# Kernel tuning notes

Hardware: AMD Instinct MI355X
Metric: run time of the kernel (lower is better)

The kernel has to match this reference:

```python
import jax, jax.numpy as jnp
import numpy as np

N, E, G = 100000, 1600000, 1000
D_IN, D, L, C = 128, 300, 5, 10


def setup_inputs() -> dict:
    key = jax.random.key(0)
    ks = jax.random.split(key, 32)
    s = 0.05
    inp = {
        'x': jax.random.normal(ks[0], (N, D_IN), jnp.float32),
        'edge_index': jax.random.randint(ks[1], (2, E), 0, N, jnp.int64),
        'batch': jnp.sort(jax.random.randint(ks[2], (N,), 0, G, jnp.int64)),
        'enc_W': jax.random.normal(ks[3], (D_IN, D)) * s,
        'enc_b': jnp.zeros((D,)),
        'eps': jnp.zeros((L,)),
        'cW1': jax.random.normal(ks[4], (L, D, 2 * D)) * s,
        'cb1': jnp.zeros((L, 2 * D)),
        'cbn_s': jnp.ones((L, 2 * D)),
        'cbn_b': jnp.zeros((L, 2 * D)),
        'cW2': jax.random.normal(ks[5], (L, 2 * D, D)) * s,
        'cb2': jnp.zeros((L, D)),
        'bn_s': jnp.ones((L, D)),
        'bn_b': jnp.zeros((L, D)),
        'vn0': jnp.zeros((D,)),
        'vW1': jax.random.normal(ks[6], (L, D, 2 * D)) * s,
        'vb1': jnp.zeros((L, 2 * D)),
        'vbn1_s': jnp.ones((L, 2 * D)),
        'vbn1_b': jnp.zeros((L, 2 * D)),
        'vW2': jax.random.normal(ks[7], (L, 2 * D, D)) * s,
        'vb2': jnp.zeros((L, D)),
        'vbn2_s': jnp.ones((L, D)),
        'vbn2_b': jnp.zeros((L, D)),
        'gW1': jax.random.normal(ks[8], (D, 2 * D)) * s,
        'gb1': jnp.zeros((2 * D,)),
        'gbn_s': jnp.ones((2 * D,)),
        'gbn_b': jnp.zeros((2 * D,)),
        'gW2': jax.random.normal(ks[9], (2 * D, 1)) * s,
        'gb2': jnp.zeros((1,)),
        'pW': jax.random.normal(ks[10], (D, C)) * s,
        'pb': jnp.zeros((C,)),
    }
    return inp


def reference(x, enc_W, enc_b, eps, cW1, cb1, cbn_s, cbn_b, cW2, cb2,
              bn_s, bn_b, vn0, vW1, vb1, vbn1_s, vbn1_b, vW2, vb2,
              vbn2_s, vbn2_b, gW1, gb1, gbn_s, gbn_b, gW2, gb2, pW, pb,
              edge_index, batch):
    src, dst = edge_index[0], edge_index[1]
    n = x.shape[0]
    vn = jnp.broadcast_to(vn0, (G, D))  # virtualnode_embedding(zeros) -> row 0 per graph
    h_list = [x @ enc_W + enc_b]
    for l in range(L):
        hl = h_list[l] + vn[batch]  # virtual-node broadcast gather
        # GIN conv: MLP((1+eps)*h + sum_{j in N(i)} h_j)
        agg = jax.ops.segment_sum(hl[src], dst, num_segments=n)
        t = (1.0 + eps[l]) * hl + agg
        t = jax.nn.relu((t @ cW1[l] + cb1[l]) * cbn_s[l] + cbn_b[l])
        h = (t @ cW2[l] + cb2[l]) * bn_s[l] + bn_b[l]  # layer BN (eval, folded)
        if l < L - 1:
            h = jax.nn.relu(h)  # dropout is identity in eval
        # virtual-node update: global_add_pool + MLP
        vtmp = jax.ops.segment_sum(hl, batch, num_segments=G) + vn
        u = jax.nn.relu((vtmp @ vW1[l] + vb1[l]) * vbn1_s[l] + vbn1_b[l])
        vn = jax.nn.relu((u @ vW2[l] + vb2[l]) * vbn2_s[l] + vbn2_b[l])
        h_list.append(h)
    # JK = 'max' across all L+1 layer outputs
    nr = jnp.max(jnp.stack(h_list, axis=0), axis=0)  # [N, D]
    # GlobalAttention pooling: gate_nn -> per-graph segment softmax
    gate = (jax.nn.relu((nr @ gW1 + gb1) * gbn_s + gbn_b) @ gW2 + gb2)[:, 0]
    gmax = jax.ops.segment_max(gate, batch, num_segments=G)
    e = jnp.exp(gate - gmax[batch])
    denom = jax.ops.segment_sum(e, batch, num_segments=G)
    alpha = e / denom[batch]
    graph_rep = jax.ops.segment_sum(nr * alpha[:, None], batch, num_segments=G)
    return graph_rep @ pW + pb  # [G, C]
```

## Files before the change

kernel.cpp:

```cpp
#include <hip/hip_runtime.h>
#include <cstddef>

#define NGRAPH 1000
#define NEDGES 1600000
#define DD     300
#define DD2    600
#define DIN    128
#define NLAYER 5
#define NCLS   10
#define BR     32
#define BRM    32

#define NT2 38
#define NK2 10
#define NT3 19
#define NK3 19
#define WFRAG 1024
#define W1F_SZ (NT2*NK2*WFRAG)

typedef unsigned short u16;
typedef unsigned char  u8;
typedef unsigned int   u32;
typedef __attribute__((ext_vector_type(8))) short short8;
typedef __attribute__((ext_vector_type(4))) short short4v;
typedef __attribute__((ext_vector_type(4))) float f32x4;

__device__ __forceinline__ u16 f2bf(float f) {
    u32 u; __builtin_memcpy(&u, &f, 4);
    u = (u + 0x7FFFu + ((u >> 16) & 1u)) >> 16;
    return (u16)u;
}
__device__ __forceinline__ float bf2f(u16 h) {
    u32 u = ((u32)h) << 16;
    float f; __builtin_memcpy(&f, &u, 4); return f;
}

__device__ __forceinline__ float ld24(const u16* __restrict__ hi, const u8* __restrict__ lo,
                                      size_t idx) {
    u32 u = ((u32)hi[idx] << 16) | ((u32)lo[idx] << 8);
    float f; __builtin_memcpy(&f, &u, 4); return f;
}
__device__ __forceinline__ void st24(u16* __restrict__ hi, u8* __restrict__ lo,
                                     size_t idx, float f) {
    u32 u; __builtin_memcpy(&u, &f, 4);
    u32 r = u + 0x7Fu + ((u >> 8) & 1u);
    hi[idx] = (u16)(r >> 16); lo[idx] = (u8)(r >> 8);
}
__device__ __forceinline__ void ld24x4(const u16* __restrict__ hi, const u8* __restrict__ lo,
                                       size_t idx, float o[4]) {
    ushort4 h = *(const ushort4*)(hi + idx);
    uchar4  l = *(const uchar4*)(lo + idx);
    u32 u0 = ((u32)h.x << 16) | ((u32)l.x << 8);
    u32 u1 = ((u32)h.y << 16) | ((u32)l.y << 8);
    u32 u2 = ((u32)h.z << 16) | ((u32)l.z << 8);
    u32 u3 = ((u32)h.w << 16) | ((u32)l.w << 8);
    __builtin_memcpy(&o[0], &u0, 4); __builtin_memcpy(&o[1], &u1, 4);
    __builtin_memcpy(&o[2], &u2, 4); __builtin_memcpy(&o[3], &u3, 4);
}
__device__ __forceinline__ void st24x4(u16* __restrict__ hi, u8* __restrict__ lo,
                                       size_t idx, const float v[4]) {
    u32 u[4];
#pragma unroll
    for (int q = 0; q < 4; ++q) {
        u32 t; __builtin_memcpy(&t, &v[q], 4);
        u[q] = t + 0x7Fu + ((t >> 8) & 1u);
    }
    ushort4 h; h.x = (u16)(u[0] >> 16); h.y = (u16)(u[1] >> 16);
    h.z = (u16)(u[2] >> 16); h.w = (u16)(u[3] >> 16);
    uchar4 l8; l8.x = (u8)(u[0] >> 8); l8.y = (u8)(u[1] >> 8);
    l8.z = (u8)(u[2] >> 8); l8.w = (u8)(u[3] >> 8);
    *(ushort4*)(hi + idx) = h;
    *(uchar4*)(lo + idx) = l8;
}

__global__ void diag_kernel(float* __restrict__ out, int n, float val)
{
    int i = blockIdx.x * 256 + threadIdx.x;
    if (i < n) out[i] = val;
}

__global__ void vn_init_kernel(float* __restrict__ vn, const float* __restrict__ vn0)
{
    int idx = blockIdx.x * 256 + threadIdx.x;
    if (idx < NGRAPH * DD) vn[idx] = vn0[idx % DD];
}

__global__ void bconv_kernel(const int* __restrict__ braw, int n, int* __restrict__ b32)
{
    int i = blockIdx.x * 256 + threadIdx.x;
    if (i >= n) return;
    int fs = (braw[n - 1] == 0) ? 2 : 1;
    b32[i] = braw[(size_t)i * fs];
}

__global__ void packW_kernel(const float* __restrict__ W, int K, int N,
                             int nT, int nK, short* __restrict__ dst)
{
    int idx = blockIdx.x * 256 + threadIdx.x;
    int total = nT * nK * 64;
    if (idx >= total) return;
    int lane = idx & 63;
    int tk = idx >> 6;
    int nn = (tk / nK) * 16 + (lane & 15);
    int k0 = (tk % nK) * 32 + (lane >> 4) * 8;
    short* o = dst + ((size_t)tk << 10) + lane * 8;
#pragma unroll
    for (int j = 0; j < 8; ++j) {
        float v = (nn < N && (k0 + j) < K) ? W[(size_t)(k0 + j) * N + nn] : 0.f;
        u16 h = f2bf(v);
        o[j] = (short)h;
        o[512 + j] = (short)f2bf(v - bf2f(h));
    }
}

__global__ void deg_kernel(const int* __restrict__ ei, int fe, int E, int* __restrict__ deg)
{
    int e = blockIdx.x * 256 + threadIdx.x;
    if (e < E) atomicAdd(&deg[ei[(size_t)fe * (E + e)]], 1);
}

__global__ void scan_kernel(const int* __restrict__ deg, int* __restrict__ row_ptr, int n)
{
    __shared__ int sd[1024];
    int t = threadIdx.x;
    int C = (n + 1023) >> 10;
    int i0 = t * C, i1 = i0 + C; if (i1 > n) i1 = n; if (i0 > n) i0 = n;
    int s = 0;
    for (int i = i0; i < i1; ++i) s += deg[i];
    sd[t] = s;
    __syncthreads();
    for (int o = 1; o < 1024; o <<= 1) {
        int x = (t >= o) ? sd[t - o] : 0;
        __syncthreads();
        sd[t] += x;
        __syncthreads();
    }
    int run = (t == 0) ? 0 : sd[t - 1];
    for (int i = i0; i < i1; ++i) { row_ptr[i] = run; run += deg[i]; }
    if (t == 1023) row_ptr[n] = sd[1023];
}

__global__ void scatter_kernel(const int* __restrict__ ei, int fe, int E,
                               int* __restrict__ cursor, int* __restrict__ col_idx)
{
    int e = blockIdx.x * 256 + threadIdx.x;
    if (e < E) {
        int d = ei[(size_t)fe * (E + e)];
        int s = ei[(size_t)fe * e];
        int p = atomicAdd(&cursor[d], 1);
        col_idx[p] = s;
    }
}

__device__ __forceinline__ int lower_bound_i(const int* __restrict__ arr, int n, int key)
{
    int lo = 0, hi = n;
    while (lo < hi) {
        int mid = (lo + hi) >> 1;
        if (arr[mid] < key) lo = mid + 1; else hi = mid;
    }
    return lo;
}

__global__ void vtmp_kernel(const u16* __restrict__ hi, const u8* __restrict__ lo,
                            const int* __restrict__ batch, const float* __restrict__ vn,
                            float* __restrict__ vtmp, int n)
{
    int g = blockIdx.x, t = threadIdx.x;
    int l0 = lower_bound_i(batch, n, g);
    int h0 = lower_bound_i(batch, n, g + 1);
    if (t >= DD) return;
    float a0 = 0.f, a1 = 0.f, a2 = 0.f, a3 = 0.f;
    int i = l0;
    for (; i + 3 < h0; i += 4) {
        a0 += ld24(hi, lo, (size_t)(i + 0) * DD + t);
        a1 += ld24(hi, lo, (size_t)(i + 1) * DD + t);
        a2 += ld24(hi, lo, (size_t)(i + 2) * DD + t);
        a3 += ld24(hi, lo, (size_t)(i + 3) * DD + t);
    }
    for (; i < h0; ++i) a0 += ld24(hi, lo, (size_t)i * DD + t);
    vtmp[(size_t)g * DD + t] = ((a0 + a1) + (a2 + a3)) + vn[(size_t)g * DD + t];
}

__global__ void vn_mlp_kernel(const float* __restrict__ vtmp,
                              const float* __restrict__ W1, const float* __restrict__ b1,
                              const float* __restrict__ s1, const float* __restrict__ sb1,
                              const float* __restrict__ W2, const float* __restrict__ b2,
                              const float* __restrict__ s2, const float* __restrict__ sb2,
                              float* __restrict__ vn)
{
    __shared__ float vt[DD];
    __shared__ float us[DD2];
    int g = blockIdx.x, t = threadIdx.x;
    if (t < DD) vt[t] = vtmp[(size_t)g * DD + t];
    __syncthreads();
    for (int j = t; j < DD2; j += 512) {
        float acc = 0.f;
        for (int k = 0; k < DD; ++k) acc = fmaf(vt[k], W1[(size_t)k * DD2 + j], acc);
        us[j] = fmaxf(fmaf(acc + b1[j], s1[j], sb1[j]), 0.f);
    }
    __syncthreads();
    for (int j = t; j < DD; j += 512) {
        float acc = 0.f;
        for (int k = 0; k < DD2; ++k) acc = fmaf(us[k], W2[(size_t)k * DD + j], acc);
        vn[(size_t)g * DD + j] = fmaxf(fmaf(acc + b2[j], s2[j], sb2[j]), 0.f);
    }
}

__global__ __launch_bounds__(1024)
void encoder_kernel(const float* __restrict__ x, const float* __restrict__ W,
                    const float* __restrict__ b,
                    u16* __restrict__ Ahi, u8* __restrict__ Alo,
                    short* __restrict__ NRm, float* __restrict__ NRscale, int n)
{
    __shared__ float xs[BR][DIN];
    __shared__ float wmax[16][8];
    __shared__ float rowS[BR];
    const int tid = threadIdx.x;
    const int base = blockIdx.x * BR;
    for (int idx = tid; idx < BR * DIN; idx += 1024) {
        int r = idx >> 7, c = idx & 127;
        int node = base + r;
        xs[r][c] = (node < n) ? x[(size_t)node * DIN + c] : 0.f;
    }
    __syncthreads();
    const int rq = tid >> 8, ct = tid & 255;
    const int wid = tid >> 6, lane = tid & 63;
    const int j0 = ct; const bool has1 = ct < (DD - 256); const int j1 = ct + 256;
    float acc[8][2] = {};
    for (int k = 0; k < DIN; ++k) {
        const float* wr = W + (size_t)k * DD;
        float w0 = wr[j0], w1 = has1 ? wr[j1] : 0.f;
#pragma unroll
        for (int i = 0; i < 8; ++i) {
            float a = xs[rq * 8 + i][k];
            acc[i][0] = fmaf(a, w0, acc[i][0]);
            acc[i][1] = fmaf(a, w1, acc[i][1]);
        }
    }
    float bb0 = b[j0], bb1 = has1 ? b[j1] : 0.f;
    float v0[8], v1[8], lm[8];
#pragma unroll
    for (int i = 0; i < 8; ++i) {
        v0[i] = acc[i][0] + bb0;
        v1[i] = has1 ? (acc[i][1] + bb1) : 0.f;
        lm[i] = fmaxf(fabsf(v0[i]), fabsf(v1[i]));
    }
#pragma unroll
    for (int o = 32; o > 0; o >>= 1)
#pragma unroll
        for (int i = 0; i < 8; ++i) lm[i] = fmaxf(lm[i], __shfl_xor(lm[i], o));
    if (lane == 0)
#pragma unroll
        for (int i = 0; i < 8; ++i) wmax[wid][i] = lm[i];
    __syncthreads();
    if (ct < 8) {
        int r = rq * 8 + ct;
        float m = fmaxf(fmaxf(wmax[4 * rq][ct], wmax[4 * rq + 1][ct]),
                        fmaxf(wmax[4 * rq + 2][ct], wmax[4 * rq + 3][ct]));
        float S = fmaxf(m, 1e-30f) / 32767.f;
        rowS[r] = S;
        if (base + r < n) NRscale[base + r] = S;
    }
    __syncthreads();
#pragma unroll
    for (int i = 0; i < 8; ++i) {
        int r = rq * 8 + i;
        int node = base + r;
        if (node >= n) continue;
        float S = rowS[r];
        size_t idx = (size_t)node * DD + j0;
        st24(Ahi, Alo, idx, v0[i]);
        NRm[idx] = (short)rintf(v0[i] / S);
        if (has1) {
            st24(Ahi, Alo, idx + 256, v1[i]);
            NRm[idx + 256] = (short)rintf(v1[i] / S);
        }
    }
}

__global__ __launch_bounds__(256)
void agg_kernel(const u16* __restrict__ Phi, const u8* __restrict__ Plo,
                u16* __restrict__ Qhi, u8* __restrict__ Qlo,
                const int* __restrict__ row_ptr, const int* __restrict__ col_idx,
                const float* __restrict__ eps, int l, int n)
{
    int node = blockIdx.x * 4 + (threadIdx.x >> 6);
    int lane = threadIdx.x & 63;
    if (node >= n) return;
    const float ep = 1.0f + eps[l];
    const bool two = (lane < 11);
    float a0[4] = {0.f, 0.f, 0.f, 0.f}, a1[4] = {0.f, 0.f, 0.f, 0.f};
    float b0[4] = {0.f, 0.f, 0.f, 0.f}, b1[4] = {0.f, 0.f, 0.f, 0.f};
    int e0 = row_ptr[node], e1 = row_ptr[node + 1];
    int e = e0;
    for (; e + 1 < e1; e += 2) {
        int s0 = col_idx[e], s1 = col_idx[e + 1];
        size_t rb0 = (size_t)s0 * DD, rb1 = (size_t)s1 * DD;
        float v[4], w[4];
        ld24x4(Phi, Plo, rb0 + lane * 4, v);
        ld24x4(Phi, Plo, rb1 + lane * 4, w);
        a0[0] += v[0]; a0[1] += v[1]; a0[2] += v[2]; a0[3] += v[3];
        b0[0] += w[0]; b0[1] += w[1]; b0[2] += w[2]; b0[3] += w[3];
        if (two) {
            ld24x4(Phi, Plo, rb0 + 256 + lane * 4, v);
            ld24x4(Phi, Plo, rb1 + 256 + lane * 4, w);
            a1[0] += v[0]; a1[1] += v[1]; a1[2] += v[2]; a1[3] += v[3];
            b1[0] += w[0]; b1[1] += w[1]; b1[2] += w[2]; b1[3] += w[3];
        }
    }
    if (e < e1) {
        int s0 = col_idx[e];
        size_t rb0 = (size_t)s0 * DD;
        float v[4];
        ld24x4(Phi, Plo, rb0 + lane * 4, v);
        a0[0] += v[0]; a0[1] += v[1]; a0[2] += v[2]; a0[3] += v[3];
        if (two) {
            ld24x4(Phi, Plo, rb0 + 256 + lane * 4, v);
            a1[0] += v[0]; a1[1] += v[1]; a1[2] += v[2]; a1[3] += v[3];
        }
    }
    size_t ob = (size_t)node * DD;
    float v[4], o[4];
    ld24x4(Phi, Plo, ob + lane * 4, v);
#pragma unroll
    for (int q = 0; q < 4; ++q) o[q] = fmaf(ep, v[q], a0[q] + b0[q]);
    st24x4(Qhi, Qlo, ob + lane * 4, o);
    if (two) {
        ld24x4(Phi, Plo, ob + 256 + lane * 4, v);
#pragma unroll
        for (int q = 0; q < 4; ++q) o[q] = fmaf(ep, v[q], a1[q] + b1[q]);
        st24x4(Qhi, Qlo, ob + 256 + lane * 4, o);
    }
}

__global__ __launch_bounds__(512)
void mlp_kernel(u16* __restrict__ Qhi, u8* __restrict__ Qlo,
                short* __restrict__ NRm, float* __restrict__ NRscale,
                const short* __restrict__ W1f, const float* __restrict__ b1,
                const float* __restrict__ s1, const float* __restrict__ sb1,
                const short* __restrict__ W2f, const float* __restrict__ b2,
                const float* __restrict__ s2, const float* __restrict__ sb2,
                int relu2, const float* __restrict__ vnp,
                const int* __restrict__ batch, int writeQ, int n)
{
    __shared__ char uni[78848];
    __shared__ float rowM[32], rowSo[32], rowSn[32];
    short* agh = (short*)uni;
    short* agl = (short*)(uni + 20992);
    short* tlh = (short*)uni;
    short* tll = (short*)(uni + 39424);
    float* outb = (float*)uni;

    const int tid = threadIdx.x;
    const int base = blockIdx.x * BRM;
    const int wv = tid >> 6, lane = tid & 63;
    const int cl = lane & 15, kq = lane >> 4, r0 = kq * 4;

    for (int idx = tid; idx < 32 * 80; idx += 512) {
        int r = idx / 80, c4 = (idx - r * 80) * 4;
        int node = base + r;
        float v[4] = {0.f, 0.f, 0.f, 0.f};
        if (c4 < DD && node < n) ld24x4(Qhi, Qlo, (size_t)node * DD + c4, v);
        short4v hh, ll;
#pragma unroll
        for (int q = 0; q < 4; ++q) {
            u16 h = f2bf(v[q]);
            hh[q] = (short)h;
            ll[q] = (short)f2bf(v[q] - bf2f(h));
        }
        *(short4v*)&agh[r * 328 + c4] = hh;
        *(short4v*)&agl[r * 328 + c4] = ll;
    }
    __syncthreads();

    {
        f32x4 acc[2][5];
#pragma unroll
        for (int s = 0; s < 2; ++s)
#pragma unroll
            for (int i = 0; i < 5; ++i) acc[s][i] = (f32x4){0.f, 0.f, 0.f, 0.f};
        const bool act5 = (wv + 32) < NT2;
        for (int ks = 0; ks < NK2; ++ks) {
            short8 bh[5], bl[5];
#pragma unroll
            for (int i = 0; i < 5; ++i) {
                int t = wv + 8 * i;
                if (i < 4 || act5) {
                    const short* bp = W1f + (((size_t)t * NK2 + ks) << 10) + lane * 8;
                    bh[i] = *(const short8*)bp;
                    bl[i] = *(const short8*)(bp + 512);
                }
            }
            short8 ah0 = *(const short8*)&agh[cl * 328 + kq * 8 + ks * 32];
            short8 al0 = *(const short8*)&agl[cl * 328 + kq * 8 + ks * 32];
            short8 ah1 = *(const short8*)&agh[(16 + cl) * 328 + kq * 8 + ks * 32];
            short8 al1 = *(const short8*)&agl[(16 + cl) * 328 + kq * 8 + ks * 32];
#pragma unroll
            for (int i = 0; i < 5; ++i)
                if (i < 4 || act5) {
                    acc[0][i] = __builtin_amdgcn_mfma_f32_16x16x32_bf16(ah0, bh[i], acc[0][i], 0, 0, 0);
                    acc[1][i] = __builtin_amdgcn_mfma_f32_16x16x32_bf16(ah1, bh[i], acc[1][i], 0, 0, 0);
                }
#pragma unroll
            for (int i = 0; i < 5; ++i)
                if (i < 4 || act5) {
                    acc[0][i] = __builtin_amdgcn_mfma_f32_16x16x32_bf16(ah0, bl[i], acc[0][i], 0, 0, 0);
                    acc[1][i] = __builtin_amdgcn_mfma_f32_16x16x32_bf16(ah1, bl[i], acc[1][i], 0, 0, 0);
                }
#pragma unroll
            for (int i = 0; i < 5; ++i)
                if (i < 4 || act5) {
                    acc[0][i] = __builtin_amdgcn_mfma_f32_16x16x32_bf16(al0, bh[i], acc[0][i], 0, 0, 0);
                    acc[1][i] = __builtin_amdgcn_mfma_f32_16x16x32_bf16(al1, bh[i], acc[1][i], 0, 0, 0);
                }
        }
        __syncthreads();
        if (tid < 256) {
            int r = tid >> 3, c = 600 + (tid & 7);
            tlh[r * 616 + c] = 0; tll[r * 616 + c] = 0;
        }
#pragma unroll
        for (int s = 0; s < 2; ++s)
#pragma unroll
            for (int i = 0; i < 5; ++i) {
                int t = wv + 8 * i;
                if (t >= NT2) continue;
                int cg = t * 16 + cl;
                if (cg < DD2) {
                    float bb = b1[cg], ss = s1[cg], cc = sb1[cg];
#pragma unroll
                    for (int r = 0; r < 4; ++r) {
                        float xv = fmaxf(fmaf(acc[s][i][r] + bb, ss, cc), 0.f);
                        u16 h = f2bf(xv);
                        tlh[(s * 16 + r0 + r) * 616 + cg] = (short)h;
                        tll[(s * 16 + r0 + r) * 616 + cg] = (short)f2bf(xv - bf2f(h));
                    }
                }
            }
    }
    __syncthreads();

    {
        f32x4 acc[2][3];
#pragma unroll
        for (int s = 0; s < 2; ++s)
#pragma unroll
            for (int i = 0; i < 3; ++i) acc[s][i] = (f32x4){0.f, 0.f, 0.f, 0.f};
        const bool act3 = (wv + 16) < NT3;
        for (int ks = 0; ks < NK3; ++ks) {
            short8 bh[3], bl[3];
#pragma unroll
            for (int i = 0; i < 3; ++i) {
                int t = wv + 8 * i;
                if (i < 2 || act3) {
                    const short* bp = W2f + (((size_t)t * NK3 + ks) << 10) + lane * 8;
                    bh[i] = *(const short8*)bp;
                    bl[i] = *(const short8*)(bp + 512);
                }
            }
            short8 ah0 = *(const short8*)&tlh[cl * 616 + kq * 8 + ks * 32];
            short8 al0 = *(const short8*)&tll[cl * 616 + kq * 8 + ks * 32];
            short8 ah1 = *(const short8*)&tlh[(16 + cl) * 616 + kq * 8 + ks * 32];
            short8 al1 = *(const short8*)&tll[(16 + cl) * 616 + kq * 8 + ks * 32];
#pragma unroll
            for (int i = 0; i < 3; ++i)
                if (i < 2 || act3) {
                    acc[0][i] = __builtin_amdgcn_mfma_f32_16x16x32_bf16(ah0, bh[i], acc[0][i], 0, 0, 0);
                    acc[1][i] = __builtin_amdgcn_mfma_f32_16x16x32_bf16(ah1, bh[i], acc[1][i], 0, 0, 0);
                }
#pragma unroll
            for (int i = 0; i < 3; ++i)
                if (i < 2 || act3) {
                    acc[0][i] = __builtin_amdgcn_mfma_f32_16x16x32_bf16(ah0, bl[i], acc[0][i], 0, 0, 0);
                    acc[1][i] = __builtin_amdgcn_mfma_f32_16x16x32_bf16(ah1, bl[i], acc[1][i], 0, 0, 0);
                }
#pragma unroll
            for (int i = 0; i < 3; ++i)
                if (i < 2 || act3) {
                    acc[0][i] = __builtin_amdgcn_mfma_f32_16x16x32_bf16(al0, bh[i], acc[0][i], 0, 0, 0);
                    acc[1][i] = __builtin_amdgcn_mfma_f32_16x16x32_bf16(al1, bh[i], acc[1][i], 0, 0, 0);
                }
        }
        __syncthreads();
#pragma unroll
        for (int s = 0; s < 2; ++s)
#pragma unroll
            for (int i = 0; i < 3; ++i) {
                int t = wv + 8 * i;
                if (t >= NT3) continue;
                int cg = t * 16 + cl;
#pragma unroll
                for (int r = 0; r < 4; ++r) outb[(s * 16 + r0 + r) * 304 + cg] = acc[s][i][r];
            }
    }
    __syncthreads();

    {
        const int rr = tid >> 4;
        const int qq = tid & 15;
        float lm = 0.f;
        for (int c = qq; c < DD; c += 16) {
            float v = fmaf(outb[rr * 304 + c] + b2[c], s2[c], sb2[c]);
            if (relu2) v = fmaxf(v, 0.f);
            outb[rr * 304 + c] = v;
            lm = fmaxf(lm, fabsf(v));
        }
#pragma unroll
        for (int o = 8; o > 0; o >>= 1) lm = fmaxf(lm, __shfl_xor(lm, o));
        if (qq == 0) rowM[rr] = lm;
    }
    __syncthreads();
    if (tid < 32) {
        int node = base + tid;
        float oS = (node < n) ? NRscale[node] : 0.f;
        float newM = fmaxf(rowM[tid], oS * 32767.f);
        float nS = fmaxf(newM, 1e-30f) / 32767.f;
        rowSo[tid] = oS; rowSn[tid] = nS;
        if (node < n) NRscale[node] = nS;
    }
    __syncthreads();
    for (int idx = tid; idx < 32 * 75; idx += 512) {
        int r = idx / 75, c = (idx - r * 75) * 4;
        int node = base + r;
        if (node >= n) continue;
        float oS = rowSo[r], inv = 1.0f / rowSn[r];
        size_t gidx = (size_t)node * DD + c;
        float h0 = outb[r * 304 + c + 0];
        float h1 = outb[r * 304 + c + 1];
        float h2 = outb[r * 304 + c + 2];
        float h3 = outb[r * 304 + c + 3];
        if (writeQ) {
            float hl[4];
            if (vnp) {
                const float* vrow = vnp + (size_t)batch[node] * DD;
                float4 vv = *(const float4*)(vrow + c);
                hl[0] = h0 + vv.x; hl[1] = h1 + vv.y; hl[2] = h2 + vv.z; hl[3] = h3 + vv.w;
            } else {
                hl[0] = h0; hl[1] = h1; hl[2] = h2; hl[3] = h3;
            }
            st24x4(Qhi, Qlo, gidx, hl);
        }
        short4v old = *(const short4v*)&NRm[gidx];
        short4v nw;
        nw[0] = (short)rintf(fmaxf((float)old[0] * oS, h0) * inv);
        nw[1] = (short)rintf(fmaxf((float)old[1] * oS, h1) * inv);
        nw[2] = (short)rintf(fmaxf((float)old[2] * oS, h2) * inv);
        nw[3] = (short)rintf(fmaxf((float)old[3] * oS, h3) * inv);
        *(short4v*)&NRm[gidx] = nw;
    }
}

__global__ __launch_bounds__(512)
void gate_kernel(const short* __restrict__ NRm, const float* __restrict__ NRscale,
                 const short* __restrict__ W1f, const float* __restrict__ b1,
                 const float* __restrict__ s1, const float* __restrict__ sb1,
                 const float* __restrict__ W2, const float* __restrict__ b2,
                 float* __restrict__ gate, int n)
{
    __shared__ char uni[78336];
    __shared__ float sc[32];
    short* nbh = (short*)uni;
    short* nbl = (short*)(uni + 20992);
    float* tlf = (float*)uni;

    const int tid = threadIdx.x;
    const int base = blockIdx.x * BRM;
    const int wv = tid >> 6, lane = tid & 63;
    const int cl = lane & 15, kq = lane >> 4, r0 = kq * 4;

    if (tid < 32) {
        int node = base + tid;
        sc[tid] = (node < n) ? NRscale[node] : 0.f;
    }
    __syncthreads();
    for (int idx = tid; idx < 32 * 80; idx += 512) {
        int r = idx / 80, c4 = (idx - r * 80) * 4;
        int node = base + r;
        float v[4] = {0.f, 0.f, 0.f, 0.f};
        if (c4 < DD && node < n) {
            short4v m4 = *(const short4v*)&NRm[(size_t)node * DD + c4];
            float s = sc[r];
            v[0] = (float)m4[0] * s; v[1] = (float)m4[1] * s;
            v[2] = (float)m4[2] * s; v[3] = (float)m4[3] * s;
        }
        short4v hh, ll;
#pragma unroll
        for (int q = 0; q < 4; ++q) {
            u16 h = f2bf(v[q]);
            hh[q] = (short)h;
            ll[q] = (short)f2bf(v[q] - bf2f(h));
        }
        *(short4v*)&nbh[r * 328 + c4] = hh;
        *(short4v*)&nbl[r * 328 + c4] = ll;
    }
    __syncthreads();

    {
        f32x4 acc[2][5];
#pragma unroll
        for (int s = 0; s < 2; ++s)
#pragma unroll
            for (int i = 0; i < 5; ++i) acc[s][i] = (f32x4){0.f, 0.f, 0.f, 0.f};
        const bool act5 = (wv + 32) < NT2;
        for (int ks = 0; ks < NK2; ++ks) {
            short8 bh[5], bl[5];
#pragma unroll
            for (int i = 0; i < 5; ++i) {
                int t = wv + 8 * i;
                if (i < 4 || act5) {
                    const short* bp = W1f + (((size_t)t * NK2 + ks) << 10) + lane * 8;
                    bh[i] = *(const short8*)bp;
                    bl[i] = *(const short8*)(bp + 512);
                }
            }
            short8 ah0 = *(const short8*)&nbh[cl * 328 + kq * 8 + ks * 32];
            short8 al0 = *(const short8*)&nbl[cl * 328 + kq * 8 + ks * 32];
            short8 ah1 = *(const short8*)&nbh[(16 + cl) * 328 + kq * 8 + ks * 32];
            short8 al1 = *(const short8*)&nbl[(16 + cl) * 328 + kq * 8 + ks * 32];
#pragma unroll
            for (int i = 0; i < 5; ++i)
                if (i < 4 || act5) {
                    acc[0][i] = __builtin_amdgcn_mfma_f32_16x16x32_bf16(ah0, bh[i], acc[0][i], 0, 0, 0);
                    acc[1][i] = __builtin_amdgcn_mfma_f32_16x16x32_bf16(ah1, bh[i], acc[1][i], 0, 0, 0);
                }
#pragma unroll
            for (int i = 0; i < 5; ++i)
                if (i < 4 || act5) {
                    acc[0][i] = __builtin_amdgcn_mfma_f32_16x16x32_bf16(ah0, bl[i], acc[0][i], 0, 0, 0);
                    acc[1][i] = __builtin_amdgcn_mfma_f32_16x16x32_bf16(ah1, bl[i], acc[1][i], 0, 0, 0);
                }
#pragma unroll
            for (int i = 0; i < 5; ++i)
                if (i < 4 || act5) {
                    acc[0][i] = __builtin_amdgcn_mfma_f32_16x16x32_bf16(al0, bh[i], acc[0][i], 0, 0, 0);
                    acc[1][i] = __builtin_amdgcn_mfma_f32_16x16x32_bf16(al1, bh[i], acc[1][i], 0, 0, 0);
                }
        }
        __syncthreads();
#pragma unroll
        for (int s = 0; s < 2; ++s)
#pragma unroll
            for (int i = 0; i < 5; ++i) {
                int t = wv + 8 * i;
                if (t >= NT2) continue;
                int cg = t * 16 + cl;
                if (cg < DD2) {
                    float bb = b1[cg], ss = s1[cg], cc = sb1[cg];
#pragma unroll
                    for (int r = 0; r < 4; ++r)
                        tlf[(s * 16 + r0 + r) * 612 + cg] = fmaxf(fmaf(acc[s][i][r] + bb, ss, cc), 0.f);
                }
            }
    }
    __syncthreads();

    {
        const int wave = tid >> 6, ln = tid & 63;
#pragma unroll
        for (int rr = 0; rr < 4; ++rr) {
            int r = wave * 4 + rr;
            int node = base + r;
            float acc = 0.f;
            for (int j = ln; j < DD2; j += 64) acc = fmaf(tlf[r * 612 + j], W2[j], acc);
#pragma unroll
            for (int o = 32; o > 0; o >>= 1) acc += __shfl_down(acc, o);
            if (ln == 0 && node < n) gate[node] = acc + b2[0];
        }
    }
}

__global__ void attn_pool_kernel(const float* __restrict__ gate,
                                 const short* __restrict__ NRm, const float* __restrict__ NRscale,
                                 const int* __restrict__ batch, float* __restrict__ rep, int n)
{
    __shared__ float red[320];
    __shared__ float bc[2];
    int g = blockIdx.x, t = threadIdx.x;
    int l0 = lower_bound_i(batch, n, g);
    int h0 = lower_bound_i(batch, n, g + 1);
    if (l0 >= h0) { if (t < DD) rep[(size_t)g * DD + t] = 0.f; return; }

    float m = -3.4e38f;
    for (int i = l0 + t; i < h0; i += 320) m = fmaxf(m, gate[i]);
    red[t] = m;
    __syncthreads();
    if (t < 64) {
        float mm = red[t];
        for (int s2 = t + 64; s2 < 320; s2 += 64) mm = fmaxf(mm, red[s2]);
#pragma unroll
        for (int o = 32; o > 0; o >>= 1) mm = fmaxf(mm, __shfl_down(mm, o));
        if (t == 0) bc[0] = mm;
    }
    __syncthreads();
    float gmax = bc[0];

    float ssum = 0.f;
    for (int i = l0 + t; i < h0; i += 320) ssum += expf(gate[i] - gmax);
    __syncthreads();
    red[t] = ssum;
    __syncthreads();
    if (t < 64) {
        float mm = red[t];
        for (int s2 = t + 64; s2 < 320; s2 += 64) mm += red[s2];
#pragma unroll
        for (int o = 32; o > 0; o >>= 1) mm += __shfl_down(mm, o);
        if (t == 0) bc[1] = mm;
    }
    __syncthreads();
    float inv = 1.0f / bc[1];

    if (t < DD) {
        float acc = 0.f;
        for (int i = l0; i < h0; ++i) {
            float w = expf(gate[i] - gmax) * inv;
            acc = fmaf(w, (float)NRm[(size_t)i * DD + t] * NRscale[i], acc);
        }
        rep[(size_t)g * DD + t] = acc;
    }
}

__global__ void final_kernel(const float* __restrict__ rep, const float* __restrict__ pW,
                             const float* __restrict__ pb, float* __restrict__ out)
{
    int g = blockIdx.x, lane = threadIdx.x;
    float a[NCLS] = {};
    for (int d = lane; d < DD; d += 64) {
        float r = rep[(size_t)g * DD + d];
#pragma unroll
        for (int c = 0; c < NCLS; ++c) a[c] = fmaf(r, pW[d * NCLS + c], a[c]);
    }
#pragma unroll
    for (int c = 0; c < NCLS; ++c) {
#pragma unroll
        for (int o = 32; o > 0; o >>= 1) a[c] += __shfl_down(a[c], o);
    }
    if (lane == 0) {
#pragma unroll
        for (int c = 0; c < NCLS; ++c) out[g * NCLS + c] = a[c] + pb[c];
    }
}

extern "C" void kernel_launch(void* const* d_in, const int* in_sizes, int n_in,
                              void* d_out, int out_size, void* d_ws, size_t ws_size,
                              hipStream_t stream)
{
    (void)n_in;
    const float* x      = (const float*)d_in[0];
    const int*   ei     = (const int*)d_in[1];
    const int*   braw   = (const int*)d_in[2];
    const float* enc_W  = (const float*)d_in[3];
    const float* enc_b  = (const float*)d_in[4];
    const float* eps    = (const float*)d_in[5];
    const float* cW1    = (const float*)d_in[6];
    const float* cb1    = (const float*)d_in[7];
    const float* cbn_s  = (const float*)d_in[8];
    const float* cbn_b  = (const float*)d_in[9];
    const float* cW2    = (const float*)d_in[10];
    const float* cb2    = (const float*)d_in[11];
    const float* bn_s   = (const float*)d_in[12];
    const float* bn_b   = (const float*)d_in[13];
    const float* vn0    = (const float*)d_in[14];
    const float* vW1    = (const float*)d_in[15];
    const float* vb1    = (const float*)d_in[16];
    const float* vbn1_s = (const float*)d_in[17];
    const float* vbn1_b = (const float*)d_in[18];
    const float* vW2    = (const float*)d_in[19];
    const float* vb2    = (const float*)d_in[20];
    const float* vbn2_s = (const float*)d_in[21];
    const float* vbn2_b = (const float*)d_in[22];
    const float* gW1    = (const float*)d_in[23];
    const float* gb1    = (const float*)d_in[24];
    const float* gbn_s  = (const float*)d_in[25];
    const float* gbn_b  = (const float*)d_in[26];
    const float* gW2    = (const float*)d_in[27];
    const float* gb2    = (const float*)d_in[28];
    const float* pW     = (const float*)d_in[29];
    const float* pb     = (const float*)d_in[30];
    float* out = (float*)d_out;

    const int N = in_sizes[0] / DIN;
    const int E = NEDGES;
    int fe = in_sizes[1] / (2 * E);
    if (fe < 1) fe = 1; if (fe > 2) fe = 2;

    char* wsp = (char*)d_ws;
    size_t off = 0;
    auto carve = [&](size_t nbytes) -> void* {
        void* p = (void*)(wsp + off);
        off += ((nbytes + 255) / 256) * 256;
        return p;
    };
    u16*   Ahi     = (u16*)  carve((size_t)N * DD * 2);
    u8*    Alo     = (u8*)   carve((size_t)N * DD);
    u16*   Bhi     = (u16*)  carve((size_t)N * DD * 2);
    u8*    Blo     = (u8*)   carve((size_t)N * DD);
    short* NRm     = (short*)carve((size_t)N * DD * 2);
    float* NRscale = (float*)carve((size_t)N * 4);
    float* vnBuf   = (float*)carve((size_t)NGRAPH * DD * 4);
    float* vtmpBuf = (float*)carve((size_t)NGRAPH * DD * 4);
    float* repBuf  = (float*)carve((size_t)NGRAPH * DD * 4);
    float* gateBuf = (float*)carve((size_t)N * 4);
    int*   batch32 = (int*)  carve((size_t)N * 4);
    int*   row_ptr = (int*)  carve(((size_t)N + 1) * 4);
    int*   cursor  = (int*)  carve((size_t)N * 4);
    int*   col_idx = (int*)  carve((size_t)E * 4);
    short* W1f     = (short*)carve((size_t)NLAYER * W1F_SZ * 2);
    short* W2f     = (short*)carve((size_t)NLAYER * W1F_SZ * 2);
    short* gW1f    = (short*)carve((size_t)W1F_SZ * 2);

    if (off > ws_size) {
        diag_kernel<<<(out_size + 255) / 256, 256, 0, stream>>>(out, out_size, (float)ws_size);
        return;
    }

    const int pkBlocks = (NT2 * NK2 * 64 + 255) / 256;
    for (int l = 0; l < NLAYER; ++l) {
        packW_kernel<<<pkBlocks, 256, 0, stream>>>(cW1 + (size_t)l * DD * DD2, DD, DD2,
                                                   NT2, NK2, W1f + (size_t)l * W1F_SZ);
        packW_kernel<<<pkBlocks, 256, 0, stream>>>(cW2 + (size_t)l * DD2 * DD, DD2, DD,
                                                   NT3, NK3, W2f + (size_t)l * W1F_SZ);
    }
    packW_kernel<<<pkBlocks, 256, 0, stream>>>(gW1, DD, DD2, NT2, NK2, gW1f);

    bconv_kernel<<<(N + 255) / 256, 256, 0, stream>>>(braw, N, batch32);

    (void)hipMemsetAsync(cursor, 0, (size_t)N * 4, stream);
    deg_kernel<<<(E + 255) / 256, 256, 0, stream>>>(ei, fe, E, cursor);
    scan_kernel<<<1, 1024, 0, stream>>>(cursor, row_ptr, N);
    (void)hipMemcpyAsync(cursor, row_ptr, (size_t)N * 4, hipMemcpyDeviceToDevice, stream);
    scatter_kernel<<<(E + 255) / 256, 256, 0, stream>>>(ei, fe, E, cursor, col_idx);

    vn_init_kernel<<<(NGRAPH * DD + 255) / 256, 256, 0, stream>>>(vnBuf, vn0);

    const int nblk32 = (N + BR - 1) / BR;
    const int nblkM  = (N + BRM - 1) / BRM;
    const int nblk4  = (N + 3) / 4;

    encoder_kernel<<<nblk32, 1024, 0, stream>>>(x, enc_W, enc_b, Ahi, Alo, NRm, NRscale, N);

    u16 *Phi = Ahi, *Qhi = Bhi; u8 *Plo = Alo, *Qlo = Blo;
    for (int l = 0; l < NLAYER; ++l) {
        const bool hasVn = (l < NLAYER - 1);
        if (hasVn)
            vtmp_kernel<<<NGRAPH, 320, 0, stream>>>(Phi, Plo, batch32, vnBuf, vtmpBuf, N);
        agg_kernel<<<nblk4, 256, 0, stream>>>(Phi, Plo, Qhi, Qlo, row_ptr, col_idx, eps, l, N);
        if (hasVn)
            vn_mlp_kernel<<<NGRAPH, 512, 0, stream>>>(
                vtmpBuf,
                vW1 + (size_t)l * DD * DD2, vb1 + (size_t)l * DD2,
                vbn1_s + (size_t)l * DD2, vbn1_b + (size_t)l * DD2,
                vW2 + (size_t)l * DD2 * DD, vb2 + (size_t)l * DD,
                vbn2_s + (size_t)l * DD, vbn2_b + (size_t)l * DD,
                vnBuf);
        mlp_kernel<<<nblkM, 512, 0, stream>>>(
            Qhi, Qlo, NRm, NRscale,
            W1f + (size_t)l * W1F_SZ, cb1 + (size_t)l * DD2,
            cbn_s + (size_t)l * DD2, cbn_b + (size_t)l * DD2,
            W2f + (size_t)l * W1F_SZ, cb2 + (size_t)l * DD,
            bn_s + (size_t)l * DD, bn_b + (size_t)l * DD,
            hasVn ? 1 : 0,
            hasVn ? vnBuf : (const float*)nullptr, batch32,
            hasVn ? 1 : 0, N);
        u16* th = Phi; Phi = Qhi; Qhi = th;
        u8*  tb = Plo; Plo = Qlo; Qlo = tb;
    }

    gate_kernel<<<nblkM, 512, 0, stream>>>(NRm, NRscale, gW1f, gb1, gbn_s, gbn_b,
                                           gW2, gb2, gateBuf, N);
    attn_pool_kernel<<<NGRAPH, 320, 0, stream>>>(gateBuf, NRm, NRscale, batch32, repBuf, N);
    final_kernel<<<NGRAPH, 64, 0, stream>>>(repBuf, pW, pb, out);
}
```

Before: 3.914 ms.

## Fuse virtual-node pooling and MLP into aggregation kernel via block specialization

```diff
diff --git a/kernel.cpp b/kernel.cpp
--- a/kernel.cpp
+++ b/kernel.cpp
@@ -160,51 +160,6 @@
         if (arr[mid] < key) lo = mid + 1; else hi = mid;
     }
     return lo;
-}
-
-__global__ void vtmp_kernel(const u16* __restrict__ hi, const u8* __restrict__ lo,
-                            const int* __restrict__ batch, const float* __restrict__ vn,
-                            float* __restrict__ vtmp, int n)
-{
-    int g = blockIdx.x, t = threadIdx.x;
-    int l0 = lower_bound_i(batch, n, g);
-    int h0 = lower_bound_i(batch, n, g + 1);
-    if (t >= DD) return;
-    float a0 = 0.f, a1 = 0.f, a2 = 0.f, a3 = 0.f;
-    int i = l0;
-    for (; i + 3 < h0; i += 4) {
-        a0 += ld24(hi, lo, (size_t)(i + 0) * DD + t);
-        a1 += ld24(hi, lo, (size_t)(i + 1) * DD + t);
-        a2 += ld24(hi, lo, (size_t)(i + 2) * DD + t);
-        a3 += ld24(hi, lo, (size_t)(i + 3) * DD + t);
-    }
-    for (; i < h0; ++i) a0 += ld24(hi, lo, (size_t)i * DD + t);
-    vtmp[(size_t)g * DD + t] = ((a0 + a1) + (a2 + a3)) + vn[(size_t)g * DD + t];
-}
-
-__global__ void vn_mlp_kernel(const float* __restrict__ vtmp,
-                              const float* __restrict__ W1, const float* __restrict__ b1,
-                              const float* __restrict__ s1, const float* __restrict__ sb1,
-                              const float* __restrict__ W2, const float* __restrict__ b2,
-                              const float* __restrict__ s2, const float* __restrict__ sb2,
-                              float* __restrict__ vn)
-{
-    __shared__ float vt[DD];
-    __shared__ float us[DD2];
-    int g = blockIdx.x, t = threadIdx.x;
-    if (t < DD) vt[t] = vtmp[(size_t)g * DD + t];
-    __syncthreads();
-    for (int j = t; j < DD2; j += 512) {
-        float acc = 0.f;
-        for (int k = 0; k < DD; ++k) acc = fmaf(vt[k], W1[(size_t)k * DD2 + j], acc);
-        us[j] = fmaxf(fmaf(acc + b1[j], s1[j], sb1[j]), 0.f);
-    }
-    __syncthreads();
-    for (int j = t; j < DD; j += 512) {
-        float acc = 0.f;
-        for (int k = 0; k < DD2; ++k) acc = fmaf(us[k], W2[(size_t)k * DD + j], acc);
-        vn[(size_t)g * DD + j] = fmaxf(fmaf(acc + b2[j], s2[j], sb2[j]), 0.f);
-    }
 }
 
 __global__ __launch_bounds__(1024)
@@ -280,12 +235,52 @@
 }
 
 __global__ __launch_bounds__(256)
-void agg_kernel(const u16* __restrict__ Phi, const u8* __restrict__ Plo,
-                u16* __restrict__ Qhi, u8* __restrict__ Qlo,
-                const int* __restrict__ row_ptr, const int* __restrict__ col_idx,
-                const float* __restrict__ eps, int l, int n)
-{
-    int node = blockIdx.x * 4 + (threadIdx.x >> 6);
+void agg_vn_kernel(const u16* __restrict__ Phi, const u8* __restrict__ Plo,
+                   u16* __restrict__ Qhi, u8* __restrict__ Qlo,
+                   const int* __restrict__ row_ptr, const int* __restrict__ col_idx,
+                   const float* __restrict__ eps, int l, int n,
+                   int vnBlocks, const int* __restrict__ batch,
+                   const float* __restrict__ vW1, const float* __restrict__ vb1,
+                   const float* __restrict__ vs1, const float* __restrict__ vsb1,
+                   const float* __restrict__ vW2, const float* __restrict__ vb2,
+                   const float* __restrict__ vs2, const float* __restrict__ vsb2,
+                   float* __restrict__ vn)
+{
+    if ((int)blockIdx.x < vnBlocks) {
+        __shared__ float vt[DD];
+        __shared__ float us[DD2];
+        const int g = blockIdx.x;
+        const int t = threadIdx.x;
+        const int l0 = lower_bound_i(batch, n, g);
+        const int h0 = lower_bound_i(batch, n, g + 1);
+        for (int c = t; c < DD; c += 256) {
+            float a0 = 0.f, a1 = 0.f, a2 = 0.f, a3 = 0.f;
+            int i = l0;
+            for (; i + 3 < h0; i += 4) {
+                a0 += ld24(Phi, Plo, (size_t)(i + 0) * DD + c);
+                a1 += ld24(Phi, Plo, (size_t)(i + 1) * DD + c);
+                a2 += ld24(Phi, Plo, (size_t)(i + 2) * DD + c);
+                a3 += ld24(Phi, Plo, (size_t)(i + 3) * DD + c);
+            }
+            for (; i < h0; ++i) a0 += ld24(Phi, Plo, (size_t)i * DD + c);
+            vt[c] = ((a0 + a1) + (a2 + a3)) + vn[(size_t)g * DD + c];
+        }
+        __syncthreads();
+        for (int j = t; j < DD2; j += 256) {
+            float acc = 0.f;
+            for (int k = 0; k < DD; ++k) acc = fmaf(vt[k], vW1[(size_t)k * DD2 + j], acc);
+            us[j] = fmaxf(fmaf(acc + vb1[j], vs1[j], vsb1[j]), 0.f);
+        }
+        __syncthreads();
+        for (int j = t; j < DD; j += 256) {
+            float acc = 0.f;
+            for (int k = 0; k < DD2; ++k) acc = fmaf(us[k], vW2[(size_t)k * DD + j], acc);
+            vn[(size_t)g * DD + j] = fmaxf(fmaf(acc + vb2[j], vs2[j], vsb2[j]), 0.f);
+        }
+        return;
+    }
+
+    int node = ((int)blockIdx.x - vnBlocks) * 4 + (threadIdx.x >> 6);
     int lane = threadIdx.x & 63;
     if (node >= n) return;
     const float ep = 1.0f + eps[l];
@@ -842,17 +837,15 @@
     u16 *Phi = Ahi, *Qhi = Bhi; u8 *Plo = Alo, *Qlo = Blo;
     for (int l = 0; l < NLAYER; ++l) {
         const bool hasVn = (l < NLAYER - 1);
-        if (hasVn)
-            vtmp_kernel<<<NGRAPH, 320, 0, stream>>>(Phi, Plo, batch32, vnBuf, vtmpBuf, N);
-        agg_kernel<<<nblk4, 256, 0, stream>>>(Phi, Plo, Qhi, Qlo, row_ptr, col_idx, eps, l, N);
-        if (hasVn)
-            vn_mlp_kernel<<<NGRAPH, 512, 0, stream>>>(
-                vtmpBuf,
-                vW1 + (size_t)l * DD * DD2, vb1 + (size_t)l * DD2,
-                vbn1_s + (size_t)l * DD2, vbn1_b + (size_t)l * DD2,
-                vW2 + (size_t)l * DD2 * DD, vb2 + (size_t)l * DD,
-                vbn2_s + (size_t)l * DD, vbn2_b + (size_t)l * DD,
-                vnBuf);
+        const int vnBlocks = hasVn ? NGRAPH : 0;
+        agg_vn_kernel<<<nblk4 + vnBlocks, 256, 0, stream>>>(
+            Phi, Plo, Qhi, Qlo, row_ptr, col_idx, eps, l, N,
+            vnBlocks, batch32,
+            vW1 + (size_t)l * DD * DD2, vb1 + (size_t)l * DD2,
+            vbn1_s + (size_t)l * DD2, vbn1_b + (size_t)l * DD2,
+            vW2 + (size_t)l * DD2 * DD, vb2 + (size_t)l * DD,
+            vbn2_s + (size_t)l * DD, vbn2_b + (size_t)l * DD,
+            vnBuf);
         mlp_kernel<<<nblkM, 512, 0, stream>>>(
             Qhi, Qlo, NRm, NRscale,
             W1f + (size_t)l * W1F_SZ, cb1 + (size_t)l * DD2,
```

Result: faster. 3.795 ms, median of 2 (-3.0%).
